# Optimization experiments

Measured on AMD Instinct MI355X. Metric: run time of the kernel, lower is better.

Reference implementation:

```python
import jax, jax.numpy as jnp
import numpy as np

B, NPG, DEG = 256, 256, 8        # graphs, nodes/graph, avg degree
IN_C, HID, OUT_C = 64, 64, 64
N = B * NPG                      # 65536 nodes
E = N * DEG                      # 524288 edges
K = NPG // 2                     # ASAP ratio=0.5 -> 128 kept nodes per graph


def setup_inputs() -> dict:
    key = jax.random.key(0)
    ks = jax.random.split(key, 12)
    x = jax.random.normal(ks[0], (N, IN_C), jnp.float32)
    # within-graph random edges, no self loops (ASAP adds remaining self loops itself)
    g = jnp.arange(E) // (NPG * DEG)
    src_l = jax.random.randint(ks[1], (E,), 0, NPG)
    off = jax.random.randint(ks[2], (E,), 1, NPG)
    dst_l = (src_l + off) % NPG
    edge_index = jnp.stack([src_l + g * NPG, dst_l + g * NPG]).astype(jnp.int32)
    batch = (jnp.arange(N) // NPG).astype(jnp.int32)
    def lin(k, fi, fo):
        return jax.random.normal(k, (fi, fo), jnp.float32) / np.sqrt(fi)
    return {
        "x": x, "edge_index": edge_index, "batch": batch,
        "W1": lin(ks[3], IN_C, HID), "b1": jnp.zeros((HID,), jnp.float32),
        "lin_W": lin(ks[4], HID, HID), "lin_b": jnp.zeros((HID,), jnp.float32),
        "att_W": lin(ks[5], 2 * HID, 1), "att_b": jnp.zeros((1,), jnp.float32),
        "le1_W": lin(ks[6], HID, 1), "le1_b": jnp.zeros((1,), jnp.float32),
        "le2_W": lin(ks[7], HID, 1),
        "le3_W": lin(ks[8], HID, 1), "le3_b": jnp.zeros((1,), jnp.float32),
        "W2": lin(ks[9], HID, OUT_C), "b2": jnp.zeros((OUT_C,), jnp.float32),
    }


def reference(x, edge_index, batch, W1, b1, lin_W, lin_b, att_W, att_b,
              le1_W, le1_b, le2_W, le3_W, le3_b, W2, b2):
    src, dst = edge_index[0], edge_index[1]
    dt = x.dtype

    # ---- conv1: GCNConv(in, hid) with self loops + symmetric norm ----
    h = x @ W1
    deg = jnp.zeros((N,), dt).at[dst].add(1.0) + 1.0  # +1 self loop
    dinv = jax.lax.rsqrt(deg)
    coef = dinv[src] * dinv[dst]
    h1 = jax.ops.segment_sum(h[src] * coef[:, None], dst, N) \
         + h * (dinv * dinv)[:, None] + b1
    h1 = jax.nn.relu(h1)  # dropout is identity at inference

    # ---- ASAPooling(hid, ratio=0.5): add remaining self loops ----
    sl = jnp.arange(N)
    srcF = jnp.concatenate([src, sl])
    dstF = jnp.concatenate([dst, sl])

    x_pool_j = h1[srcF]                                   # [Ef, HID]
    x_q = jax.ops.segment_max(x_pool_j, dstF, N)          # master-node max
    x_q = (x_q @ lin_W + lin_b)[dstF]
    s = (jnp.concatenate([x_q, x_pool_j], axis=-1) @ att_W + att_b)[:, 0]
    s = jax.nn.leaky_relu(s, 0.2)
    # segment softmax over edges grouped by target
    smax = jax.ops.segment_max(s, dstF, N)
    e = jnp.exp(s - smax[dstF])
    score = e / (jax.ops.segment_sum(e, dstF, N) + 1e-16)[dstF]
    xnew = jax.ops.segment_sum(h1[srcF] * score[:, None], dstF, N)

    # fitness = sigmoid(LEConv(xnew, edges_with_self_loops))
    # LEConv: out_i = sum_{j->i}(lin1(x_j) - lin2(x_i)) + lin3(x_i)
    a = xnew @ le1_W + le1_b
    b2_ = xnew @ le2_W
    degF = jnp.zeros((N,), dt).at[dstF].add(1.0)
    fit = jax.ops.segment_sum(a[srcF], dstF, N)[:, 0] - degF * b2_[:, 0] \
          + (xnew @ le3_W + le3_b)[:, 0]
    fitness = jax.nn.sigmoid(fit)

    # top-k (ratio=0.5) per graph; equal contiguous graphs -> static shapes
    _, topi = jax.lax.top_k(fitness.reshape(B, NPG), K)   # [B, K]
    perm = (topi + jnp.arange(B)[:, None] * NPG).reshape(-1)
    x_sel = xnew[perm] * fitness[perm][:, None]           # [B*K, HID]

    # graph coarsening: A' = S^T A S (dense per graph), diag removed
    g_e = dstF // NPG
    sL = srcF - g_e * NPG
    dL = dstF - g_e * NPG
    A = jnp.zeros((B, NPG, NPG), dt).at[g_e, sL, dL].add(1.0)
    S = jnp.zeros((B, NPG, NPG), dt).at[g_e, sL, dL].add(score)
    Ssel = jnp.take_along_axis(S, topi[:, None, :], axis=2)   # [B, NPG, K]
    AS = jnp.einsum('bij,bjk->bik', A, Ssel)                  # A @ S
    A2 = jnp.einsum('bji,bjk->bik', Ssel, AS)                 # S^T (A S) -> [B,K,K]
    A2 = A2 * (1.0 - jnp.eye(K, dtype=dt))                    # remove_diag

    # ---- conv2: GCNConv(hid, out); returned edge_weight is discarded in
    # the original forward, so edges are binary (nnz of A') + self loops ----
    M = (A2 > 0).astype(dt) + jnp.eye(K, dtype=dt)            # [B, src, dst]
    h2 = (x_sel @ W2).reshape(B, K, OUT_C)
    deg2 = M.sum(axis=1)                                      # in-degree per target
    d2 = jax.lax.rsqrt(deg2)
    Mn = M * d2[:, :, None] * d2[:, None, :]
    out2 = jnp.einsum('bsd,bsf->bdf', Mn, h2) + b2            # [B, K, OUT_C]

    # ---- global_mean_pool over each graph's K kept nodes ----
    return out2.mean(axis=1)                                  # [B, OUT_C]
```

## Files before the change

kernel.cpp:

```cpp
#include <hip/hip_runtime.h>

typedef float f4 __attribute__((ext_vector_type(4)));
typedef unsigned long long u64;

#define NPGL 256
#define EPGL 2048
#define HIDD 64
#define KKEEP 128
#define NTH 1024
#define RSTR 72

__device__ __forceinline__ int ro(int n, int c) { return n * RSTR + c * 4; }

__global__ void __launch_bounds__(NTH)
asap_fused(const float* __restrict__ x, const int* __restrict__ ei,
           const float* __restrict__ W1, const float* __restrict__ b1,
           const float* __restrict__ linW, const float* __restrict__ linb,
           const float* __restrict__ attW, const float* __restrict__ attb,
           const float* __restrict__ le1W, const float* __restrict__ le1b,
           const float* __restrict__ le2W,
           const float* __restrict__ le3W, const float* __restrict__ le3b,
           const float* __restrict__ W2, const float* __restrict__ b2,
           float* __restrict__ out, int Etot)
{
  const int g = blockIdx.x;
  const int tid = threadIdx.x;

  __shared__ __align__(16) float buf[NPGL * RSTR];
  __shared__ __align__(16) float mskf[4096];
  __shared__ __align__(16) float esc[EPGL];
  __shared__ __align__(8) unsigned char csrc[4096];
  __shared__ unsigned short rowstU[NPGL + 1];
  __shared__ unsigned short rowstP[NPGL + 1];
  __shared__ int cnt[NPGL];
  __shared__ float dinv_[NPGL];
  __shared__ float sA[NPGL], sB[NPGL];
  __shared__ float rsf[NPGL];
  __shared__ float u_[HIDD], wsum[HIDD];
  __shared__ int scanw[4], scanwP[4];
  __shared__ float c0s;

  u64* Imask = (u64*)mskf;
  u64* Rmask = ((u64*)mskf) + 1024;
  u64* conn  = ((u64*)mskf) + 1536;
  int*   kept = (int*)(mskf + 3584);
  float* d2A  = mskf + 3712;
  float* cA   = mskf + 3840;

  const int ebase = g * EPGL;
  const int nbase = g * NPGL;

  ((u64*)mskf)[tid] = 0ull;
  if (tid < NPGL) { cnt[tid] = 0; ((u64*)mskf)[1536 + tid] = 0ull; }
  __syncthreads();

  int es[2], ed[2];
#pragma unroll
  for (int i = 0; i < 2; ++i) {
    const int e = tid + i * NTH;
    es[i] = ei[ebase + e] - nbase;
    ed[i] = ei[Etot + ebase + e] - nbase;
    atomicAdd(&cnt[ed[i]], 1);
  }
  {
    const f4* xg = (const f4*)(x + (size_t)nbase * HIDD);
#pragma unroll
    for (int ii = 0; ii < 4; ++ii) {
      const int i = tid + ii * NTH;
      *(f4*)&buf[ro(i >> 4, i & 15)] = xg[i];
    }
  }
  __syncthreads();

  int sU = 0, sP = 0, mU = 0;
  if (tid < NPGL) {
    mU = cnt[tid];
    const int mP = (mU + 7) & ~7;
    sU = mU; sP = mP;
#pragma unroll
    for (int off = 1; off < 64; off <<= 1) {
      const int uU = __shfl_up(sU, off, 64);
      const int uP = __shfl_up(sP, off, 64);
      if ((tid & 63) >= off) { sU += uU; sP += uP; }
    }
    if ((tid & 63) == 63) { scanw[tid >> 6] = sU; scanwP[tid >> 6] = sP; }
  }
  __syncthreads();
  if (tid < NPGL) {
    int aU = 0, aP = 0;
    const int w = tid >> 6;
    for (int ww = 0; ww < w; ++ww) { aU += scanw[ww]; aP += scanwP[ww]; }
    rowstU[tid + 1] = (unsigned short)(sU + aU);
    rowstP[tid + 1] = (unsigned short)(sP + aP);
    if (tid == 0) { rowstU[0] = 0; rowstP[0] = 0; }
    cnt[tid] = 0;
    dinv_[tid] = rsqrtf((float)mU + 1.0f);
  }
  if (tid < HIDD) {
    float a = 0.f;
    for (int f = 0; f < HIDD; ++f) a += linW[tid * HIDD + f] * attW[f];
    u_[tid] = a;
  }
  if (tid == 0) {
    float a = 0.f;
    for (int f = 0; f < HIDD; ++f) a += linb[f] * attW[f];
    c0s = a + attb[0];
  }
  __syncthreads();

#pragma unroll
  for (int i = 0; i < 2; ++i) {
    const int j = atomicAdd(&cnt[ed[i]], 1);
    csrc[(int)rowstP[ed[i]] + j] = (unsigned char)es[i];
  }
  if (tid < NPGL) atomicOr(&Imask[tid * 4 + (tid >> 6)], 1ull << (tid & 63));
#pragma unroll
  for (int i = 0; i < 2; ++i)
    atomicOr(&Imask[ed[i] * 4 + (es[i] >> 6)], 1ull << (es[i] & 63));
  __syncthreads();

  {
    const int wv = tid >> 6;
    const int r  = ((wv & 3) << 6) + (tid & 63);
    const int fc = __builtin_amdgcn_readfirstlane(wv >> 2);
    const float* __restrict__ Wg = W1 + fc * 16;
    f4 acc[4];
#pragma unroll
    for (int c = 0; c < 4; ++c) acc[c] = f4{0.f, 0.f, 0.f, 0.f};
#pragma unroll
    for (int p = 0; p < 4; ++p) {
      f4 xa[4];
#pragma unroll
      for (int c = 0; c < 4; ++c) xa[c] = *(const f4*)&buf[ro(r, p * 4 + c)];
#pragma unroll
      for (int kk = 0; kk < 16; ++kk) {
        const int k = p * 16 + kk;
        const float xv = ((const float*)xa)[kk];
        const float* __restrict__ Wk = Wg + k * HIDD;
#pragma unroll
        for (int c = 0; c < 4; ++c)
          acc[c] += xv * *(const f4*)(Wk + c * 4);
      }
    }
    const float dv = dinv_[r];
    __syncthreads();
#pragma unroll
    for (int c = 0; c < 4; ++c) *(f4*)&buf[ro(r, fc * 4 + c)] = acc[c] * dv;
  }
  __syncthreads();

  {
    const int d = tid >> 2, hh = tid & 3;
    const float dd = dinv_[d];
    const int deg = cnt[d];
    const int p0 = rowstP[d];
    const int hb = ro(0, hh);
    f4 acc[4], acc2[4];
#pragma unroll
    for (int j = 0; j < 4; ++j) {
      acc[j] = *(const f4*)&buf[ro(d, hh) + j * 16];
      acc2[j] = f4{0.f, 0.f, 0.f, 0.f};
    }
    const int nb = deg >> 3;
    int j8 = 0;
    for (int b = 0; b < nb; ++b, j8 += 8) {
      const u64 bits = *(const u64*)(csrc + p0 + j8);
#pragma unroll
      for (int t = 0; t < 8; ++t) {
        const int s = (int)((bits >> (8 * t)) & 255);
        const int base = s * RSTR + hb;
        if (t & 1) {
#pragma unroll
          for (int j = 0; j < 4; ++j) acc2[j] += *(const f4*)&buf[base + j * 16];
        } else {
#pragma unroll
          for (int j = 0; j < 4; ++j) acc[j] += *(const f4*)&buf[base + j * 16];
        }
      }
    }
    const int rem = deg & 7;
    if (rem) {
      const u64 bits = *(const u64*)(csrc + p0 + j8);
      for (int t = 0; t < rem; ++t) {
        const int s = (int)((bits >> (8 * t)) & 255);
        const int base = s * RSTR + hb;
#pragma unroll
        for (int j = 0; j < 4; ++j) acc[j] += *(const f4*)&buf[base + j * 16];
      }
    }
    float sBp = 0.f;
#pragma unroll
    for (int j = 0; j < 4; ++j) {
      acc[j] = (acc[j] + acc2[j]) * dd + *(const f4*)&b1[4 * (hh + 4 * j)];
      acc[j] = __builtin_elementwise_max(acc[j], f4{0.f, 0.f, 0.f, 0.f});
      const f4 aw = *(const f4*)&attW[HIDD + 4 * (hh + 4 * j)];
      sBp += acc[j].x * aw.x + acc[j].y * aw.y + acc[j].z * aw.z + acc[j].w * aw.w;
    }
    sBp += __shfl_xor(sBp, 1); sBp += __shfl_xor(sBp, 2);
    if (hh == 0) sB[d] = sBp;
    __syncthreads();
#pragma unroll
    for (int j = 0; j < 4; ++j) *(f4*)&buf[ro(d, hh) + j * 16] = acc[j];
  }
  __syncthreads();

  {
    const int d = tid >> 2, hh = tid & 3;
    const int deg = cnt[d];
    const int p0 = rowstP[d];
    const int q0 = rowstU[d];
    const int hb = hh * 4;
    f4 own[4], mx[4], mx2[4];
#pragma unroll
    for (int j = 0; j < 4; ++j) {
      own[j] = *(const f4*)&buf[ro(d, hh) + j * 16];
      mx[j] = own[j];
      mx2[j] = own[j];
    }
    const int nb = deg >> 3;
    int j8 = 0;
    for (int b = 0; b < nb; ++b, j8 += 8) {
      const u64 bits = *(const u64*)(csrc + p0 + j8);
#pragma unroll
      for (int t = 0; t < 8; ++t) {
        const int s = (int)((bits >> (8 * t)) & 255);
        const int base = s * RSTR + hb;
        if (t & 1) {
#pragma unroll
          for (int j = 0; j < 4; ++j)
            mx2[j] = __builtin_elementwise_max(mx2[j], *(const f4*)&buf[base + j * 16]);
        } else {
#pragma unroll
          for (int j = 0; j < 4; ++j)
            mx[j] = __builtin_elementwise_max(mx[j], *(const f4*)&buf[base + j * 16]);
        }
      }
    }
    const int rem = deg & 7;
    if (rem) {
      const u64 bits = *(const u64*)(csrc + p0 + j8);
      for (int t = 0; t < rem; ++t) {
        const int s = (int)((bits >> (8 * t)) & 255);
        const int base = s * RSTR + hb;
#pragma unroll
        for (int j = 0; j < 4; ++j)
          mx[j] = __builtin_elementwise_max(mx[j], *(const f4*)&buf[base + j * 16]);
      }
    }
    float sAv = 0.f;
#pragma unroll
    for (int j = 0; j < 4; ++j) {
      mx[j] = __builtin_elementwise_max(mx[j], mx2[j]);
      const f4 uu = *(const f4*)&u_[4 * (hh + 4 * j)];
      sAv += mx[j].x * uu.x + mx[j].y * uu.y + mx[j].z * uu.z + mx[j].w * uu.w;
    }
    sAv += __shfl_xor(sAv, 1); sAv += __shfl_xor(sAv, 2);
    const float sa = c0s + sAv;
    const float sBd = sB[d];
    float mxB = sBd;
#pragma unroll 4
    for (int t = hh; t < deg; t += 4) mxB = fmaxf(mxB, sB[csrc[p0 + t]]);
    mxB = fmaxf(mxB, __shfl_xor(mxB, 1));
    mxB = fmaxf(mxB, __shfl_xor(mxB, 2));
    float mxv = sa + mxB;
    mxv = mxv >= 0.f ? mxv : 0.2f * mxv;
    float sum = 0.f;
#pragma unroll 4
    for (int t = hh; t < deg; t += 4) {
      float sc = sa + sB[csrc[p0 + t]];
      sc = sc >= 0.f ? sc : 0.2f * sc;
      const float e = __expf(sc - mxv);
      esc[q0 + t] = e;
      sum += e;
    }
    sum += __shfl_xor(sum, 1); sum += __shfl_xor(sum, 2);
    float scS = sa + sBd;
    scS = scS >= 0.f ? scS : 0.2f * scS;
    const float esf = __expf(scS - mxv);
    const float rs = 1.0f / (esf + sum + 1e-16f);
    asm volatile("s_waitcnt lgkmcnt(0)" ::: "memory");
    f4 a[4], a2[4];
#pragma unroll
    for (int j = 0; j < 4; ++j) { a[j] = esf * own[j]; a2[j] = f4{0.f, 0.f, 0.f, 0.f}; }
    j8 = 0;
    for (int b = 0; b < nb; ++b, j8 += 8) {
      const u64 bits = *(const u64*)(csrc + p0 + j8);
#pragma unroll
      for (int t = 0; t < 8; ++t) {
        const int s = (int)((bits >> (8 * t)) & 255);
        const float e = esc[q0 + j8 + t];
        const int base = s * RSTR + hb;
        if (t & 1) {
#pragma unroll
          for (int j = 0; j < 4; ++j) a2[j] += e * *(const f4*)&buf[base + j * 16];
        } else {
#pragma unroll
          for (int j = 0; j < 4; ++j) a[j] += e * *(const f4*)&buf[base + j * 16];
        }
      }
    }
    if (rem) {
      const u64 bits = *(const u64*)(csrc + p0 + j8);
      for (int t = 0; t < rem; ++t) {
        const int s = (int)((bits >> (8 * t)) & 255);
        const float e = esc[q0 + j8 + t];
        const int base = s * RSTR + hb;
#pragma unroll
        for (int j = 0; j < 4; ++j) a[j] += e * *(const f4*)&buf[base + j * 16];
      }
    }
#pragma unroll
    for (int j = 0; j < 4; ++j) a[j] = (a[j] + a2[j]) * rs;
    __syncthreads();
#pragma unroll
    for (int j = 0; j < 4; ++j) *(f4*)&buf[ro(d, hh) + j * 16] = a[j];
  }
  __syncthreads();

  {
    const int n = tid >> 2, q = tid & 3;
    float av = 0.f, bv = 0.f, cv = 0.f;
#pragma unroll
    for (int j = 0; j < 4; ++j) {
      const int c = q + 4 * j;
      const f4 v = *(const f4*)&buf[ro(n, q) + j * 16];
      const int k = c * 4;
      av += v.x * le1W[k] + v.y * le1W[k + 1] + v.z * le1W[k + 2] + v.w * le1W[k + 3];
      bv += v.x * le2W[k] + v.y * le2W[k + 1] + v.z * le2W[k + 2] + v.w * le2W[k + 3];
      cv += v.x * le3W[k] + v.y * le3W[k + 1] + v.z * le3W[k + 2] + v.w * le3W[k + 3];
    }
    av += __shfl_xor(av, 1); av += __shfl_xor(av, 2);
    bv += __shfl_xor(bv, 1); bv += __shfl_xor(bv, 2);
    cv += __shfl_xor(cv, 1); cv += __shfl_xor(cv, 2);
    if (q == 0) {
      sA[n] = av + le1b[0];
      sB[n] = bv;
      dinv_[n] = cv + le3b[0];
    }
  }
  __syncthreads();
  {
    const int d = tid >> 2, q = tid & 3;
    const int deg = cnt[d];
    const int p0 = rowstP[d];
    float fp = 0.f;
#pragma unroll 4
    for (int t = q; t < deg; t += 4) fp += sA[csrc[p0 + t]];
    fp += __shfl_xor(fp, 1); fp += __shfl_xor(fp, 2);
    if (q == 0) {
      float f = sA[d] + fp;
      f -= (float)(deg + 1) * sB[d];
      f += dinv_[d];
      float sg;
      if (f >= 0.f) sg = 1.f / (1.f + expf(-f));
      else { const float t2 = expf(f); sg = t2 / (1.f + t2); }
      rsf[d] = sg;
    }
  }
  __syncthreads();

  {
    const int n = tid >> 2, q = tid & 3;
    const float fn = rsf[n];
    int r = 0;
    for (int m = q * 64; m < q * 64 + 64; ++m) {
      const float fm = rsf[m];
      r += ((fm > fn) || (fm == fn && m < n)) ? 1 : 0;
    }
    r += __shfl_xor(r, 1); r += __shfl_xor(r, 2);
    if (q == 0 && r < KKEEP) kept[r] = n;
  }
  __syncthreads();

  if (tid < KKEEP * 4) {
    const int q = tid >> 2, w = tid & 3;
    const int kq = kept[q];
    u64 acc = 0ull;
#pragma unroll
    for (int ww = 0; ww < 4; ++ww) {
      u64 bits = Imask[kq * 4 + ww];
      while (bits) {
        const int m = (ww << 6) + __builtin_ctzll(bits);
        bits &= bits - 1;
        acc |= Imask[m * 4 + w];
      }
    }
    Rmask[q * 4 + w] = acc;
  }
  __syncthreads();
  if (tid < KKEEP * 4) {
    const int p = tid >> 2, wb = tid & 3;
    const int kp = kept[p];
    const u64 I0 = Imask[kp * 4 + 0], I1 = Imask[kp * 4 + 1],
              I2 = Imask[kp * 4 + 2], I3 = Imask[kp * 4 + 3];
    u64 bits = 0ull;
    for (int j = 0; j < 32; ++j) {
      const int q = wb * 32 + j;
      if (q == p) continue;
      const u64* R = &Rmask[q * 4];
      if ((I0 & R[0]) | (I1 & R[1]) | (I2 & R[2]) | (I3 & R[3]))
        bits |= 1ull << (q & 63);
    }
    atomicOr(&conn[p * 2 + (wb >> 1)], bits);
  }
  __syncthreads();

  if (tid < KKEEP * 4) {
    const int q = tid >> 2, h = tid & 3;
    const int w = q >> 6, sh = q & 63;
    int c = 0;
    for (int p = h * 32; p < h * 32 + 32; ++p)
      c += (int)((conn[p * 2 + w] >> sh) & 1ull);
    c += __shfl_xor(c, 1); c += __shfl_xor(c, 2);
    if (h == 0) d2A[q] = rsqrtf((float)(c + 1));
  }
  __syncthreads();
  if (tid < KKEEP * 4) {
    const int s = tid >> 2, h = tid & 3;
    unsigned int b32 = (unsigned int)(conn[s * 2 + (h >> 1)] >> (32 * (h & 1)));
    const int base = ((h >> 1) << 6) + ((h & 1) << 5);
    float acc = 0.f;
    while (b32) {
      const int d_ = base + __builtin_ctz(b32);
      b32 &= b32 - 1;
      acc += d2A[d_];
    }
    acc += __shfl_xor(acc, 1); acc += __shfl_xor(acc, 2);
    if (h == 0)
      cA[s] = d2A[s] * (d2A[s] + acc) * rsf[kept[s]] * (1.0f / (float)KKEEP);
  }
  __syncthreads();

  {
    const int f = tid & 63, blk = tid >> 6;
    float p = 0.f;
    for (int j = 0; j < 8; ++j) {
      const int s = blk * 8 + j;
      const int ks = kept[s];
      p += cA[s] * buf[ks * RSTR + f];
    }
    esc[blk * 64 + f] = p;
  }
  __syncthreads();
  if (tid < HIDD) {
    float s = 0.f;
#pragma unroll
    for (int b = 0; b < 16; ++b) s += esc[b * 64 + tid];
    wsum[tid] = s;
  }
  __syncthreads();
  if (tid < HIDD) {
    float o = b2[tid];
    for (int k = 0; k < HIDD; ++k) o += wsum[k] * W2[k * HIDD + tid];
    out[(size_t)g * HIDD + tid] = o;
  }
}

extern "C" void kernel_launch(void* const* d_in, const int* in_sizes, int n_in,
                              void* d_out, int out_size, void* d_ws, size_t ws_size,
                              hipStream_t stream) {
  (void)n_in; (void)out_size; (void)d_ws; (void)ws_size;
  const float* x    = (const float*)d_in[0];
  const int*   ei   = (const int*)d_in[1];
  const float* W1   = (const float*)d_in[3];
  const float* b1   = (const float*)d_in[4];
  const float* linW = (const float*)d_in[5];
  const float* linb = (const float*)d_in[6];
  const float* attW = (const float*)d_in[7];
  const float* attb = (const float*)d_in[8];
  const float* le1W = (const float*)d_in[9];
  const float* le1b = (const float*)d_in[10];
  const float* le2W = (const float*)d_in[11];
  const float* le3W = (const float*)d_in[12];
  const float* le3b = (const float*)d_in[13];
  const float* W2   = (const float*)d_in[14];
  const float* b2   = (const float*)d_in[15];
  const int Etot = in_sizes[1] / 2;
  const int nGraphs = 256;

  asap_fused<<<dim3(nGraphs), dim3(NTH), 0, stream>>>(
      x, ei, W1, b1, linW, linb, attW, attb, le1W, le1b, le2W, le3W, le3b,
      W2, b2, (float*)d_out, Etot);
}
```

Baseline: 51.31 us.

## Load x directly into registers, cache CSR neighbor bytes in registers across stages

The node features are now read straight from global memory into registers for the W1 matmul, so the LDS staging pass and one block barrier go away. The CSR build is overlapped with that load. The first 32 neighbor indices of each node are kept in registers and reused across the aggregation, max, softmax and score stages, and the unpadded row-start array is dropped in favour of the padded offsets. This removes repeated LDS index reads and a scan, but raises register pressure through the 16 f4 x values and the cached index words, and enlarges the esc buffer.

```diff
diff --git a/kernel.cpp b/kernel.cpp
--- a/kernel.cpp
+++ b/kernel.cpp
@@ -28,16 +28,15 @@
 
   __shared__ __align__(16) float buf[NPGL * RSTR];
   __shared__ __align__(16) float mskf[4096];
-  __shared__ __align__(16) float esc[EPGL];
+  __shared__ __align__(16) float esc[4096];
   __shared__ __align__(8) unsigned char csrc[4096];
-  __shared__ unsigned short rowstU[NPGL + 1];
   __shared__ unsigned short rowstP[NPGL + 1];
   __shared__ int cnt[NPGL];
   __shared__ float dinv_[NPGL];
   __shared__ float sA[NPGL], sB[NPGL];
   __shared__ float rsf[NPGL];
   __shared__ float u_[HIDD], wsum[HIDD];
-  __shared__ int scanw[4], scanwP[4];
+  __shared__ int scanwP[4];
   __shared__ float c0s;
 
   u64* Imask = (u64*)mskf;
@@ -62,37 +61,26 @@
     ed[i] = ei[Etot + ebase + e] - nbase;
     atomicAdd(&cnt[ed[i]], 1);
   }
-  {
-    const f4* xg = (const f4*)(x + (size_t)nbase * HIDD);
-#pragma unroll
-    for (int ii = 0; ii < 4; ++ii) {
-      const int i = tid + ii * NTH;
-      *(f4*)&buf[ro(i >> 4, i & 15)] = xg[i];
-    }
-  }
-  __syncthreads();
-
-  int sU = 0, sP = 0, mU = 0;
+  __syncthreads();
+
+  int sP = 0, mU = 0;
   if (tid < NPGL) {
     mU = cnt[tid];
-    const int mP = (mU + 7) & ~7;
-    sU = mU; sP = mP;
+    sP = (mU + 7) & ~7;
 #pragma unroll
     for (int off = 1; off < 64; off <<= 1) {
-      const int uU = __shfl_up(sU, off, 64);
       const int uP = __shfl_up(sP, off, 64);
-      if ((tid & 63) >= off) { sU += uU; sP += uP; }
-    }
-    if ((tid & 63) == 63) { scanw[tid >> 6] = sU; scanwP[tid >> 6] = sP; }
+      if ((tid & 63) >= off) sP += uP;
+    }
+    if ((tid & 63) == 63) scanwP[tid >> 6] = sP;
   }
   __syncthreads();
   if (tid < NPGL) {
-    int aU = 0, aP = 0;
+    int aP = 0;
     const int w = tid >> 6;
-    for (int ww = 0; ww < w; ++ww) { aU += scanw[ww]; aP += scanwP[ww]; }
-    rowstU[tid + 1] = (unsigned short)(sU + aU);
+    for (int ww = 0; ww < w; ++ww) aP += scanwP[ww];
     rowstP[tid + 1] = (unsigned short)(sP + aP);
-    if (tid == 0) { rowstU[0] = 0; rowstP[0] = 0; }
+    if (tid == 0) rowstP[0] = 0;
     cnt[tid] = 0;
     dinv_[tid] = rsqrtf((float)mU + 1.0f);
   }
@@ -108,80 +96,92 @@
   }
   __syncthreads();
 
-#pragma unroll
-  for (int i = 0; i < 2; ++i) {
-    const int j = atomicAdd(&cnt[ed[i]], 1);
-    csrc[(int)rowstP[ed[i]] + j] = (unsigned char)es[i];
-  }
-  if (tid < NPGL) atomicOr(&Imask[tid * 4 + (tid >> 6)], 1ull << (tid & 63));
-#pragma unroll
-  for (int i = 0; i < 2; ++i)
-    atomicOr(&Imask[ed[i] * 4 + (es[i] >> 6)], 1ull << (es[i] & 63));
-  __syncthreads();
-
-  {
+  {
+#pragma unroll
+    for (int i = 0; i < 2; ++i) {
+      const int j = atomicAdd(&cnt[ed[i]], 1);
+      csrc[(int)rowstP[ed[i]] + j] = (unsigned char)es[i];
+    }
+    if (tid < NPGL) atomicOr(&Imask[tid * 4 + (tid >> 6)], 1ull << (tid & 63));
+#pragma unroll
+    for (int i = 0; i < 2; ++i)
+      atomicOr(&Imask[ed[i] * 4 + (es[i] >> 6)], 1ull << (es[i] & 63));
+
     const int wv = tid >> 6;
     const int r  = ((wv & 3) << 6) + (tid & 63);
     const int fc = __builtin_amdgcn_readfirstlane(wv >> 2);
     const float* __restrict__ Wg = W1 + fc * 16;
+    const f4* __restrict__ xg = (const f4*)(x + (size_t)(nbase + r) * HIDD);
+    f4 xa[16];
+#pragma unroll
+    for (int c = 0; c < 16; ++c) xa[c] = xg[c];
     f4 acc[4];
 #pragma unroll
     for (int c = 0; c < 4; ++c) acc[c] = f4{0.f, 0.f, 0.f, 0.f};
 #pragma unroll
-    for (int p = 0; p < 4; ++p) {
-      f4 xa[4];
-#pragma unroll
-      for (int c = 0; c < 4; ++c) xa[c] = *(const f4*)&buf[ro(r, p * 4 + c)];
-#pragma unroll
-      for (int kk = 0; kk < 16; ++kk) {
-        const int k = p * 16 + kk;
-        const float xv = ((const float*)xa)[kk];
-        const float* __restrict__ Wk = Wg + k * HIDD;
-#pragma unroll
-        for (int c = 0; c < 4; ++c)
-          acc[c] += xv * *(const f4*)(Wk + c * 4);
-      }
+    for (int k = 0; k < HIDD; ++k) {
+      const float xv = ((const float*)xa)[k];
+      const float* __restrict__ Wk = Wg + k * HIDD;
+#pragma unroll
+      for (int c = 0; c < 4; ++c)
+        acc[c] += xv * *(const f4*)(Wk + c * 4);
     }
     const float dv = dinv_[r];
-    __syncthreads();
 #pragma unroll
     for (int c = 0; c < 4; ++c) *(f4*)&buf[ro(r, fc * 4 + c)] = acc[c] * dv;
   }
   __syncthreads();
 
-  {
-    const int d = tid >> 2, hh = tid & 3;
+  const int d = tid >> 2, hh = tid & 3;
+  const int deg = cnt[d];
+  const int p0 = rowstP[d];
+  const int hb = hh * 4;
+  u64 ib[4];
+#pragma unroll
+  for (int b = 0; b < 4; ++b)
+    ib[b] = (b * 8 < deg) ? *(const u64*)(csrc + p0 + b * 8) : 0ull;
+
+  {
     const float dd = dinv_[d];
-    const int deg = cnt[d];
-    const int p0 = rowstP[d];
-    const int hb = ro(0, hh);
     f4 acc[4], acc2[4];
 #pragma unroll
     for (int j = 0; j < 4; ++j) {
-      acc[j] = *(const f4*)&buf[ro(d, hh) + j * 16];
+      acc[j] = *(const f4*)&buf[d * RSTR + hb + j * 16];
       acc2[j] = f4{0.f, 0.f, 0.f, 0.f};
     }
-    const int nb = deg >> 3;
-    int j8 = 0;
-    for (int b = 0; b < nb; ++b, j8 += 8) {
+#pragma unroll
+    for (int b = 0; b < 4; ++b) {
+      const int base8 = b * 8;
+      if (base8 < deg) {
+        const u64 bits = ib[b];
+        if (deg - base8 >= 8) {
+#pragma unroll
+          for (int t = 0; t < 8; ++t) {
+            const int s = (int)((bits >> (8 * t)) & 255);
+            const int base = s * RSTR + hb;
+            if (t & 1) {
+#pragma unroll
+              for (int j = 0; j < 4; ++j) acc2[j] += *(const f4*)&buf[base + j * 16];
+            } else {
+#pragma unroll
+              for (int j = 0; j < 4; ++j) acc[j] += *(const f4*)&buf[base + j * 16];
+            }
+          }
+        } else {
+          const int lim = deg - base8;
+          for (int t = 0; t < lim; ++t) {
+            const int s = (int)((bits >> (8 * t)) & 255);
+            const int base = s * RSTR + hb;
+#pragma unroll
+            for (int j = 0; j < 4; ++j) acc[j] += *(const f4*)&buf[base + j * 16];
+          }
+        }
+      }
+    }
+    for (int j8 = 32; j8 < deg; j8 += 8) {
       const u64 bits = *(const u64*)(csrc + p0 + j8);
-#pragma unroll
-      for (int t = 0; t < 8; ++t) {
-        const int s = (int)((bits >> (8 * t)) & 255);
-        const int base = s * RSTR + hb;
-        if (t & 1) {
-#pragma unroll
-          for (int j = 0; j < 4; ++j) acc2[j] += *(const f4*)&buf[base + j * 16];
-        } else {
-#pragma unroll
-          for (int j = 0; j < 4; ++j) acc[j] += *(const f4*)&buf[base + j * 16];
-        }
-      }
-    }
-    const int rem = deg & 7;
-    if (rem) {
-      const u64 bits = *(const u64*)(csrc + p0 + j8);
-      for (int t = 0; t < rem; ++t) {
+      const int lim = (deg - j8 >= 8) ? 8 : deg - j8;
+      for (int t = 0; t < lim; ++t) {
         const int s = (int)((bits >> (8 * t)) & 255);
         const int base = s * RSTR + hb;
 #pragma unroll
@@ -200,46 +200,53 @@
     if (hh == 0) sB[d] = sBp;
     __syncthreads();
 #pragma unroll
-    for (int j = 0; j < 4; ++j) *(f4*)&buf[ro(d, hh) + j * 16] = acc[j];
-  }
-  __syncthreads();
-
-  {
-    const int d = tid >> 2, hh = tid & 3;
-    const int deg = cnt[d];
-    const int p0 = rowstP[d];
-    const int q0 = rowstU[d];
-    const int hb = hh * 4;
-    f4 own[4], mx[4], mx2[4];
+    for (int j = 0; j < 4; ++j) *(f4*)&buf[d * RSTR + hb + j * 16] = acc[j];
+  }
+  __syncthreads();
+
+  {
+    f4 mx[4], mx2[4];
 #pragma unroll
     for (int j = 0; j < 4; ++j) {
-      own[j] = *(const f4*)&buf[ro(d, hh) + j * 16];
-      mx[j] = own[j];
-      mx2[j] = own[j];
-    }
-    const int nb = deg >> 3;
-    int j8 = 0;
-    for (int b = 0; b < nb; ++b, j8 += 8) {
+      mx[j] = *(const f4*)&buf[d * RSTR + hb + j * 16];
+      mx2[j] = mx[j];
+    }
+#pragma unroll
+    for (int b = 0; b < 4; ++b) {
+      const int base8 = b * 8;
+      if (base8 < deg) {
+        const u64 bits = ib[b];
+        if (deg - base8 >= 8) {
+#pragma unroll
+          for (int t = 0; t < 8; ++t) {
+            const int s = (int)((bits >> (8 * t)) & 255);
+            const int base = s * RSTR + hb;
+            if (t & 1) {
+#pragma unroll
+              for (int j = 0; j < 4; ++j)
+                mx2[j] = __builtin_elementwise_max(mx2[j], *(const f4*)&buf[base + j * 16]);
+            } else {
+#pragma unroll
+              for (int j = 0; j < 4; ++j)
+                mx[j] = __builtin_elementwise_max(mx[j], *(const f4*)&buf[base + j * 16]);
+            }
+          }
+        } else {
+          const int lim = deg - base8;
+          for (int t = 0; t < lim; ++t) {
+            const int s = (int)((bits >> (8 * t)) & 255);
+            const int base = s * RSTR + hb;
+#pragma unroll
+            for (int j = 0; j < 4; ++j)
+              mx[j] = __builtin_elementwise_max(mx[j], *(const f4*)&buf[base + j * 16]);
+          }
+        }
+      }
+    }
+    for (int j8 = 32; j8 < deg; j8 += 8) {
       const u64 bits = *(const u64*)(csrc + p0 + j8);
-#pragma unroll
-      for (int t = 0; t < 8; ++t) {
-        const int s = (int)((bits >> (8 * t)) & 255);
-        const int base = s * RSTR + hb;
-        if (t & 1) {
-#pragma unroll
-          for (int j = 0; j < 4; ++j)
-            mx2[j] = __builtin_elementwise_max(mx2[j], *(const f4*)&buf[base + j * 16]);
-        } else {
-#pragma unroll
-          for (int j = 0; j < 4; ++j)
-            mx[j] = __builtin_elementwise_max(mx[j], *(const f4*)&buf[base + j * 16]);
-        }
-      }
-    }
-    const int rem = deg & 7;
-    if (rem) {
-      const u64 bits = *(const u64*)(csrc + p0 + j8);
-      for (int t = 0; t < rem; ++t) {
+      const int lim = (deg - j8 >= 8) ? 8 : deg - j8;
+      for (int t = 0; t < lim; ++t) {
         const int s = (int)((bits >> (8 * t)) & 255);
         const int base = s * RSTR + hb;
 #pragma unroll
@@ -256,21 +263,41 @@
     }
     sAv += __shfl_xor(sAv, 1); sAv += __shfl_xor(sAv, 2);
     const float sa = c0s + sAv;
+
     const float sBd = sB[d];
+    float rc[8];
+#pragma unroll
+    for (int i = 0; i < 8; ++i) {
+      const int t = hh + 4 * i;
+      rc[i] = (t < deg)
+                ? sB[(int)((ib[i >> 1] >> (8 * hh + 32 * (i & 1))) & 255)]
+                : -1e30f;
+    }
     float mxB = sBd;
-#pragma unroll 4
-    for (int t = hh; t < deg; t += 4) mxB = fmaxf(mxB, sB[csrc[p0 + t]]);
+#pragma unroll
+    for (int i = 0; i < 8; ++i) mxB = fmaxf(mxB, rc[i]);
+    for (int t = 32 + hh; t < deg; t += 4) mxB = fmaxf(mxB, sB[csrc[p0 + t]]);
     mxB = fmaxf(mxB, __shfl_xor(mxB, 1));
     mxB = fmaxf(mxB, __shfl_xor(mxB, 2));
     float mxv = sa + mxB;
     mxv = mxv >= 0.f ? mxv : 0.2f * mxv;
     float sum = 0.f;
-#pragma unroll 4
-    for (int t = hh; t < deg; t += 4) {
+#pragma unroll
+    for (int i = 0; i < 8; ++i) {
+      const int t = hh + 4 * i;
+      if (t < deg) {
+        float sc = sa + rc[i];
+        sc = sc >= 0.f ? sc : 0.2f * sc;
+        const float e = __expf(sc - mxv);
+        esc[p0 + t] = e;
+        sum += e;
+      }
+    }
+    for (int t = 32 + hh; t < deg; t += 4) {
       float sc = sa + sB[csrc[p0 + t]];
       sc = sc >= 0.f ? sc : 0.2f * sc;
       const float e = __expf(sc - mxv);
-      esc[q0 + t] = e;
+      esc[p0 + t] = e;
       sum += e;
     }
     sum += __shfl_xor(sum, 1); sum += __shfl_xor(sum, 2);
@@ -279,32 +306,54 @@
     const float esf = __expf(scS - mxv);
     const float rs = 1.0f / (esf + sum + 1e-16f);
     asm volatile("s_waitcnt lgkmcnt(0)" ::: "memory");
+
     f4 a[4], a2[4];
 #pragma unroll
-    for (int j = 0; j < 4; ++j) { a[j] = esf * own[j]; a2[j] = f4{0.f, 0.f, 0.f, 0.f}; }
-    j8 = 0;
-    for (int b = 0; b < nb; ++b, j8 += 8) {
+    for (int j = 0; j < 4; ++j) {
+      a[j] = esf * *(const f4*)&buf[d * RSTR + hb + j * 16];
+      a2[j] = f4{0.f, 0.f, 0.f, 0.f};
+    }
+#pragma unroll
+    for (int b = 0; b < 4; ++b) {
+      const int base8 = b * 8;
+      if (base8 < deg) {
+        const u64 bits = ib[b];
+        if (deg - base8 >= 8) {
+          const f4 e0 = *(const f4*)&esc[p0 + base8];
+          const f4 e1 = *(const f4*)&esc[p0 + base8 + 4];
+          const float ev[8] = {e0.x, e0.y, e0.z, e0.w, e1.x, e1.y, e1.z, e1.w};
+#pragma unroll
+          for (int t = 0; t < 8; ++t) {
+            const int s = (int)((bits >> (8 * t)) & 255);
+            const int base = s * RSTR + hb;
+            const float e = ev[t];
+            if (t & 1) {
+#pragma unroll
+              for (int j = 0; j < 4; ++j) a2[j] += e * *(const f4*)&buf[base + j * 16];
+            } else {
+#pragma unroll
+              for (int j = 0; j < 4; ++j) a[j] += e * *(const f4*)&buf[base + j * 16];
+            }
+          }
+        } else {
+          const int lim = deg - base8;
+          for (int t = 0; t < lim; ++t) {
+            const int s = (int)((bits >> (8 * t)) & 255);
+            const int base = s * RSTR + hb;
+            const float e = esc[p0 + base8 + t];
+#pragma unroll
+            for (int j = 0; j < 4; ++j) a[j] += e * *(const f4*)&buf[base + j * 16];
+          }
+        }
+      }
+    }
+    for (int j8 = 32; j8 < deg; j8 += 8) {
       const u64 bits = *(const u64*)(csrc + p0 + j8);
-#pragma unroll
-      for (int t = 0; t < 8; ++t) {
+      const int lim = (deg - j8 >= 8) ? 8 : deg - j8;
+      for (int t = 0; t < lim; ++t) {
         const int s = (int)((bits >> (8 * t)) & 255);
-        const float e = esc[q0 + j8 + t];
         const int base = s * RSTR + hb;
-        if (t & 1) {
-#pragma unroll
-          for (int j = 0; j < 4; ++j) a2[j] += e * *(const f4*)&buf[base + j * 16];
-        } else {
-#pragma unroll
-          for (int j = 0; j < 4; ++j) a[j] += e * *(const f4*)&buf[base + j * 16];
-        }
-      }
-    }
-    if (rem) {
-      const u64 bits = *(const u64*)(csrc + p0 + j8);
-      for (int t = 0; t < rem; ++t) {
-        const int s = (int)((bits >> (8 * t)) & 255);
-        const float e = esc[q0 + j8 + t];
-        const int base = s * RSTR + hb;
+        const float e = esc[p0 + j8 + t];
 #pragma unroll
         for (int j = 0; j < 4; ++j) a[j] += e * *(const f4*)&buf[base + j * 16];
       }
@@ -313,17 +362,16 @@
     for (int j = 0; j < 4; ++j) a[j] = (a[j] + a2[j]) * rs;
     __syncthreads();
 #pragma unroll
-    for (int j = 0; j < 4; ++j) *(f4*)&buf[ro(d, hh) + j * 16] = a[j];
-  }
-  __syncthreads();
-
-  {
-    const int n = tid >> 2, q = tid & 3;
+    for (int j = 0; j < 4; ++j) *(f4*)&buf[d * RSTR + hb + j * 16] = a[j];
+  }
+  __syncthreads();
+
+  {
     float av = 0.f, bv = 0.f, cv = 0.f;
 #pragma unroll
     for (int j = 0; j < 4; ++j) {
-      const int c = q + 4 * j;
-      const f4 v = *(const f4*)&buf[ro(n, q) + j * 16];
+      const int c = hh + 4 * j;
+      const f4 v = *(const f4*)&buf[d * RSTR + hb + j * 16];
       const int k = c * 4;
       av += v.x * le1W[k] + v.y * le1W[k + 1] + v.z * le1W[k + 2] + v.w * le1W[k + 3];
       bv += v.x * le2W[k] + v.y * le2W[k + 1] + v.z * le2W[k + 2] + v.w * le2W[k + 3];
@@ -332,22 +380,24 @@
     av += __shfl_xor(av, 1); av += __shfl_xor(av, 2);
     bv += __shfl_xor(bv, 1); bv += __shfl_xor(bv, 2);
     cv += __shfl_xor(cv, 1); cv += __shfl_xor(cv, 2);
-    if (q == 0) {
-      sA[n] = av + le1b[0];
-      sB[n] = bv;
-      dinv_[n] = cv + le3b[0];
-    }
-  }
-  __syncthreads();
-  {
-    const int d = tid >> 2, q = tid & 3;
-    const int deg = cnt[d];
-    const int p0 = rowstP[d];
+    if (hh == 0) {
+      sA[d] = av + le1b[0];
+      sB[d] = bv;
+      dinv_[d] = cv + le3b[0];
+    }
+  }
+  __syncthreads();
+  {
     float fp = 0.f;
-#pragma unroll 4
-    for (int t = q; t < deg; t += 4) fp += sA[csrc[p0 + t]];
+#pragma unroll
+    for (int i = 0; i < 8; ++i) {
+      const int t = hh + 4 * i;
+      if (t < deg)
+        fp += sA[(int)((ib[i >> 1] >> (8 * hh + 32 * (i & 1))) & 255)];
+    }
+    for (int t = 32 + hh; t < deg; t += 4) fp += sA[csrc[p0 + t]];
     fp += __shfl_xor(fp, 1); fp += __shfl_xor(fp, 2);
-    if (q == 0) {
+    if (hh == 0) {
       float f = sA[d] + fp;
       f -= (float)(deg + 1) * sB[d];
       f += dinv_[d];
@@ -360,15 +410,14 @@
   __syncthreads();
 
   {
-    const int n = tid >> 2, q = tid & 3;
-    const float fn = rsf[n];
+    const float fn = rsf[d];
     int r = 0;
-    for (int m = q * 64; m < q * 64 + 64; ++m) {
+    for (int m = hh * 64; m < hh * 64 + 64; ++m) {
       const float fm = rsf[m];
-      r += ((fm > fn) || (fm == fn && m < n)) ? 1 : 0;
+      r += ((fm > fn) || (fm == fn && m < d)) ? 1 : 0;
     }
     r += __shfl_xor(r, 1); r += __shfl_xor(r, 2);
-    if (q == 0 && r < KKEEP) kept[r] = n;
+    if (hh == 0 && r < KKEEP) kept[r] = d;
   }
   __syncthreads();
 
```

Measured after the change: 66.72 us. 30.0% more time.
